# Kernel optimization log

Hardware: AMD Instinct MI355X
Metric: run time of the kernel (lower is better)

The kernel has to match this reference:

```python
import jax, jax.numpy as jnp
import numpy as np

B, S, D, H = 4, 2048, 1024, 16
HD = D // H  # head_dim = 64


def setup_inputs() -> dict:
    key = jax.random.key(0)
    ks = jax.random.split(key, 6)
    sd = 1.0 / np.sqrt(D)
    return {
        "x": jax.random.normal(ks[0], (B, S, D), dtype=jnp.float32),
        "y": jax.random.normal(ks[1], (B, S, D), dtype=jnp.float32),
        "mask": jax.random.normal(ks[2], (1, 1, S, S), dtype=jnp.float32),
        "Wkv": jax.random.normal(ks[3], (D, 2 * D), dtype=jnp.float32) * sd,
        "bkv": jnp.zeros((2 * D,), dtype=jnp.float32),
        "Wq": jax.random.normal(ks[4], (D, D), dtype=jnp.float32) * sd,
        "bq": jnp.zeros((D,), dtype=jnp.float32),
        "Wo": jax.random.normal(ks[5], (D, D), dtype=jnp.float32) * sd,
        "bo": jnp.zeros((D,), dtype=jnp.float32),
    }


def reference(x, y, mask, Wkv, bkv, Wq, bq, Wo, bo):
    b, s, d = x.shape
    kv = x @ Wkv + bkv                      # [B,S,2D]
    q = y @ Wq + bq                         # [B,S,D]
    kv = kv.reshape(b, s, H, 2 * HD).transpose(0, 2, 1, 3)  # [B,H,S,2HD]
    q = q.reshape(b, s, H, HD).transpose(0, 2, 1, 3)        # [B,H,S,HD]
    k, v = kv[..., :HD], kv[..., HD:]
    scaled = jnp.einsum("bhqd,bhkd->bhqk", q, k) / jnp.sqrt(jnp.float32(HD))
    scaled = scaled + mask                  # additive mask, broadcast [1,1,S,S]
    attn = jax.nn.softmax(scaled, axis=-1)
    vals = jnp.einsum("bhqk,bhkd->bhqd", attn, v)  # [B,H,S,HD]
    vals = vals.transpose(0, 2, 1, 3).reshape(b, s, d)
    return vals @ Wo + bo
```

## Files before the change

kernel.cpp:

```cpp
#include <hip/hip_runtime.h>

#define LOG2E 1.44269504088896340736f
#define QSCALE 0.18033688011112042f

typedef __attribute__((ext_vector_type(8))) short bf16x8;
typedef __attribute__((ext_vector_type(4))) float f32x4;

__device__ __forceinline__ unsigned short f2b(float f) {
  union { float f; unsigned int u; } x; x.f = f;
  return (unsigned short)((x.u + 0x8000u) >> 16);
}

__device__ __forceinline__ unsigned int pk_bf16(float a, float b) {
  union { float f; unsigned int u; } xa, xb; xa.f = a; xb.f = b;
  return __builtin_amdgcn_perm(xb.u + 0x8000u, xa.u + 0x8000u, 0x07060302);
}

__device__ __forceinline__ void gld_lds16(const void* g, void* l) {
  __builtin_amdgcn_global_load_lds((const __attribute__((address_space(1))) void*)g,
                                   (__attribute__((address_space(3))) void*)l,
                                   16, 0, 0);
}

__global__ __launch_bounds__(256) void cast_xy(const float* __restrict__ x,
                                               const float* __restrict__ y,
                                               unsigned short* __restrict__ xb,
                                               unsigned short* __restrict__ yb) {
  int i = blockIdx.x * 256 + threadIdx.x;
  const float* in = x; unsigned short* out = xb;
  if (i >= 2097152) { in = y; out = yb; i -= 2097152; }
  float4 v = ((const float4*)in)[i];
  uint2 o;
  o.x = pk_bf16(v.x, v.y);
  o.y = pk_bf16(v.z, v.w);
  ((uint2*)out)[i] = o;
}

__global__ __launch_bounds__(256) void scale_mask(const float* __restrict__ in,
                                                  float* __restrict__ out) {
  int i = blockIdx.x * 256 + threadIdx.x;
  f32x4 v = ((const f32x4*)in)[i];
  ((f32x4*)out)[i] = v * LOG2E;
}

__global__ __launch_bounds__(256) void transpose_cast_all(
    const float* __restrict__ Wkv, const float* __restrict__ Wq,
    const float* __restrict__ Wo, unsigned short* __restrict__ wkvt,
    unsigned short* __restrict__ wqt, unsigned short* __restrict__ wot) {
  __shared__ float t[32][33];
  int tb = blockIdx.x;
  const float* W; unsigned short* Wt; int N;
  if (tb < 2048)      { W = Wkv; Wt = wkvt; N = 2048; }
  else if (tb < 3072) { W = Wq;  Wt = wqt;  N = 1024; tb -= 2048; }
  else                { W = Wo;  Wt = wot;  N = 1024; tb -= 3072; }
  const int K = 1024;
  int tilesN = N >> 5;
  int nb = (tb % tilesN) * 32, kb = (tb / tilesN) * 32;
  int j = threadIdx.x & 31, i0 = threadIdx.x >> 5;
  #pragma unroll
  for (int p = 0; p < 4; ++p) {
    int i = i0 + p * 8;
    t[i][j] = W[(size_t)(kb + i) * N + nb + j];
  }
  __syncthreads();
  #pragma unroll
  for (int p = 0; p < 4; ++p) {
    int i = i0 + p * 8;
    Wt[(size_t)(nb + i) * K + kb + j] = f2b(t[j][i]);
  }
}

template <int MODE>
__global__ __launch_bounds__(256)
void gemm128(const unsigned short* __restrict__ A,
             const unsigned short* __restrict__ Bt,
             const float* __restrict__ bias,
             void* __restrict__ out0, void* __restrict__ out1,
             int M, int N, int K) {
  __shared__ __align__(16) unsigned short As[128 * 64];
  __shared__ __align__(16) unsigned short Bs[128 * 64];
  const int tid = threadIdx.x;
  const int bn = blockIdx.x, bm = blockIdx.y;
  const int wave = tid >> 6, lane = tid & 63;
  const int wm = (wave >> 1) * 64, wn = (wave & 1) * 64;
  const int lrow = lane & 15, quad = lane >> 4;
  const int sw = lrow & 7;

  f32x4 acc[4][4];
  #pragma unroll
  for (int i = 0; i < 4; ++i)
    #pragma unroll
    for (int j = 0; j < 4; ++j)
      #pragma unroll
      for (int r = 0; r < 4; ++r) acc[i][j][r] = 0.f;

  const unsigned short* Ab = A + (size_t)(bm * 128) * K;
  const unsigned short* Bb = Bt + (size_t)(bn * 128) * K;

  for (int k0 = 0; k0 < K; k0 += 64) {
    #pragma unroll
    for (int i = 0; i < 4; ++i) {
      int e = i * 256 + tid;
      int row = e >> 3, gs = (e & 7) ^ (row & 7);
      gld_lds16(Ab + (size_t)row * K + k0 + gs * 8, &As[e * 8]);
    }
    #pragma unroll
    for (int i = 0; i < 4; ++i) {
      int e = i * 256 + tid;
      int row = e >> 3, gs = (e & 7) ^ (row & 7);
      gld_lds16(Bb + (size_t)row * K + k0 + gs * 8, &Bs[e * 8]);
    }
    __builtin_amdgcn_s_waitcnt(0);
    __syncthreads();
    #pragma unroll
    for (int ks = 0; ks < 2; ++ks) {
      bf16x8 af[4], bf[4];
      const int g = ((ks * 4 + quad) ^ sw) * 8;
      #pragma unroll
      for (int i = 0; i < 4; ++i)
        af[i] = *(const bf16x8*)&As[(wm + i * 16 + lrow) * 64 + g];
      #pragma unroll
      for (int j = 0; j < 4; ++j)
        bf[j] = *(const bf16x8*)&Bs[(wn + j * 16 + lrow) * 64 + g];
      #pragma unroll
      for (int i = 0; i < 4; ++i)
        #pragma unroll
        for (int j = 0; j < 4; ++j)
          acc[i][j] = __builtin_amdgcn_mfma_f32_16x16x32_bf16(af[i], bf[j], acc[i][j], 0, 0, 0);
    }
    __syncthreads();
  }

  const int col0 = bn * 128 + wn;
  #pragma unroll
  for (int i = 0; i < 4; ++i) {
    const int row0 = bm * 128 + wm + i * 16 + quad * 4;
    const int b = row0 >> 11, s0 = row0 & 2047;
    #pragma unroll
    for (int j = 0; j < 4; ++j) {
      const int cc = j * 16 + lrow;
      const float bv = bias[col0 + cc];
      float v0 = acc[i][j][0] + bv, v1 = acc[i][j][1] + bv;
      float v2 = acc[i][j][2] + bv, v3 = acc[i][j][3] + bv;
      if (MODE == 0) {
        float* C = (float*)out0;
        size_t off = (size_t)row0 * N + col0 + cc;
        C[off] = v0; C[off + N] = v1; C[off + 2 * N] = v2; C[off + 3 * N] = v3;
      } else if (MODE == 1) {
        const int h = col0 >> 7;
        if ((col0 & 64) == 0) {
          unsigned short* Kb = (unsigned short*)out0;
          size_t base = ((size_t)(b * 16 + h) * 2048 + s0) * 64 + cc;
          Kb[base] = f2b(v0); Kb[base + 64] = f2b(v1);
          Kb[base + 128] = f2b(v2); Kb[base + 192] = f2b(v3);
        } else {
          unsigned short* Vt = (unsigned short*)out1;
          size_t base = ((size_t)(b * 16 + h) * 64 + cc) * 2048 + s0;
          uint2 p; p.x = pk_bf16(v0, v1); p.y = pk_bf16(v2, v3);
          *(uint2*)&Vt[base] = p;
        }
      } else {
        v0 *= QSCALE; v1 *= QSCALE; v2 *= QSCALE; v3 *= QSCALE;
        const int h = col0 >> 6;
        unsigned short* Qb = (unsigned short*)out0;
        size_t base = ((size_t)(b * 16 + h) * 2048 + s0) * 64 + cc;
        Qb[base] = f2b(v0); Qb[base + 64] = f2b(v1);
        Qb[base + 128] = f2b(v2); Qb[base + 192] = f2b(v3);
      }
    }
  }
}

__global__ __launch_bounds__(256)
void attn(const unsigned short* __restrict__ Qbuf,
          const unsigned short* __restrict__ Kbuf,
          const unsigned short* __restrict__ Vtbuf,
          const float* __restrict__ masks,
          unsigned short* __restrict__ vals) {
  const int blk = blockIdx.x;
  const int xcd = blk & 7, slot = blk >> 3;
  const int qt = xcd * 2 + (slot >> 6);
  const int hb = slot & 63;
  const int b = hb >> 4, h = hb & 15;
  const int tid = threadIdx.x, lane = tid & 63, w = tid >> 6;
  const int lrow = lane & 15, quad = lane >> 4;
  const int sw = lrow & 7;

  __shared__ __align__(16) unsigned short Ks[64 * 64];
  __shared__ __align__(16) unsigned short Vs[64 * 64];
  __shared__ __align__(16) unsigned short Ps[128 * 72];

  const unsigned short* qp = Qbuf + ((size_t)(b * 16 + h) * 2048 + qt * 128) * 64;
  const unsigned short* kp = Kbuf + (size_t)(b * 16 + h) * 2048 * 64;
  const unsigned short* vp = Vtbuf + (size_t)(b * 16 + h) * 64 * 2048;
  const float* mp = masks + (size_t)(qt * 128 + w * 32) * 2048;

  #pragma unroll
  for (int i = 0; i < 4; ++i) {
    int e = i * 256 + tid;
    int row = e >> 3, gs = (e & 7) ^ (row & 7);
    gld_lds16(qp + (size_t)row * 64 + gs * 8, &Ps[e * 8]);
  }
  __builtin_amdgcn_s_waitcnt(0);
  __syncthreads();
  bf16x8 qf[2][2];
  #pragma unroll
  for (int iq = 0; iq < 2; ++iq)
    #pragma unroll
    for (int ks = 0; ks < 2; ++ks)
      qf[iq][ks] = *(const bf16x8*)&Ps[(w * 32 + iq * 16 + lrow) * 64 + ((ks * 4 + quad) ^ sw) * 8];
  __syncthreads();

  f32x4 o_acc[4][2];
  #pragma unroll
  for (int id = 0; id < 4; ++id)
    #pragma unroll
    for (int iq = 0; iq < 2; ++iq)
      #pragma unroll
      for (int r = 0; r < 4; ++r) o_acc[id][iq][r] = 0.f;
  float lsum[2] = {0.f, 0.f};

  for (int kt = 0; kt < 32; ++kt) {
    __syncthreads();
    #pragma unroll
    for (int i = 0; i < 2; ++i) {
      int e = i * 256 + tid;
      int row = e >> 3, gs = (e & 7) ^ (row & 7);
      gld_lds16(kp + (size_t)(kt * 64 + row) * 64 + gs * 8, &Ks[e * 8]);
    }
    #pragma unroll
    for (int i = 0; i < 2; ++i) {
      int e = i * 256 + tid;
      int row = e >> 3, gs = (e & 7) ^ (row & 7);
      gld_lds16(vp + (size_t)row * 2048 + kt * 64 + gs * 8, &Vs[e * 8]);
    }
    __builtin_amdgcn_s_waitcnt(0);
    __syncthreads();

    f32x4 z[4][2];
    #pragma unroll
    for (int ik = 0; ik < 4; ++ik)
      #pragma unroll
      for (int iq = 0; iq < 2; ++iq)
        z[ik][iq] = *(const f32x4*)(mp + (size_t)(iq * 16 + lrow) * 2048 + kt * 64 + ik * 16 + quad * 4);

    #pragma unroll
    for (int ks = 0; ks < 2; ++ks) {
      bf16x8 kf[4];
      const int g = ((ks * 4 + quad) ^ sw) * 8;
      #pragma unroll
      for (int ik = 0; ik < 4; ++ik)
        kf[ik] = *(const bf16x8*)&Ks[(ik * 16 + lrow) * 64 + g];
      #pragma unroll
      for (int ik = 0; ik < 4; ++ik)
        #pragma unroll
        for (int iq = 0; iq < 2; ++iq)
          z[ik][iq] = __builtin_amdgcn_mfma_f32_16x16x32_bf16(kf[ik], qf[iq][ks], z[ik][iq], 0, 0, 0);
    }

    #pragma unroll
    for (int ik = 0; ik < 4; ++ik)
      #pragma unroll
      for (int iq = 0; iq < 2; ++iq) {
        float e0 = exp2f(z[ik][iq][0]), e1 = exp2f(z[ik][iq][1]);
        float e2 = exp2f(z[ik][iq][2]), e3 = exp2f(z[ik][iq][3]);
        lsum[iq] += (e0 + e1) + (e2 + e3);
        uint2 p;
        p.x = pk_bf16(e0, e1);
        p.y = pk_bf16(e2, e3);
        *(uint2*)&Ps[(w * 32 + iq * 16 + lrow) * 72 + ik * 16 + quad * 4] = p;
      }
    __builtin_amdgcn_s_waitcnt(0xC07F);

    #pragma unroll
    for (int ks = 0; ks < 2; ++ks) {
      bf16x8 vf[4], pf[2];
      const int g = ((ks * 4 + quad) ^ sw) * 8;
      #pragma unroll
      for (int id = 0; id < 4; ++id)
        vf[id] = *(const bf16x8*)&Vs[(id * 16 + lrow) * 64 + g];
      #pragma unroll
      for (int iq = 0; iq < 2; ++iq)
        pf[iq] = *(const bf16x8*)&Ps[(w * 32 + iq * 16 + lrow) * 72 + ks * 32 + quad * 8];
      #pragma unroll
      for (int id = 0; id < 4; ++id)
        #pragma unroll
        for (int iq = 0; iq < 2; ++iq)
          o_acc[id][iq] = __builtin_amdgcn_mfma_f32_16x16x32_bf16(vf[id], pf[iq], o_acc[id][iq], 0, 0, 0);
    }
  }

  unsigned short* ob = vals + (size_t)(b * 2048 + qt * 128 + w * 32) * 1024 + h * 64;
  #pragma unroll
  for (int iq = 0; iq < 2; ++iq) {
    float s = lsum[iq];
    s += __shfl_xor(s, 16);
    s += __shfl_xor(s, 32);
    float inv = 1.f / s;
    #pragma unroll
    for (int id = 0; id < 4; ++id) {
      uint2 p;
      p.x = pk_bf16(o_acc[id][iq][0] * inv, o_acc[id][iq][1] * inv);
      p.y = pk_bf16(o_acc[id][iq][2] * inv, o_acc[id][iq][3] * inv);
      *(uint2*)&ob[(size_t)(iq * 16 + lrow) * 1024 + id * 16 + quad * 4] = p;
    }
  }
}

extern "C" void kernel_launch(void* const* d_in, const int* in_sizes, int n_in,
                              void* d_out, int out_size, void* d_ws, size_t ws_size,
                              hipStream_t stream) {
  const float* x    = (const float*)d_in[0];
  const float* y    = (const float*)d_in[1];
  const float* mask = (const float*)d_in[2];
  const float* Wkv  = (const float*)d_in[3];
  const float* bkv  = (const float*)d_in[4];
  const float* Wq   = (const float*)d_in[5];
  const float* bq   = (const float*)d_in[6];
  const float* Wo   = (const float*)d_in[7];
  const float* bo   = (const float*)d_in[8];

  char* ws = (char*)d_ws;
  unsigned short* xb    = (unsigned short*)(ws + ((size_t)0 << 20));
  unsigned short* yb    = (unsigned short*)(ws + ((size_t)16 << 20));
  unsigned short* wkvt  = (unsigned short*)(ws + ((size_t)32 << 20));
  unsigned short* wqt   = (unsigned short*)(ws + ((size_t)36 << 20));
  unsigned short* wot   = (unsigned short*)(ws + ((size_t)38 << 20));
  unsigned short* kbuf  = (unsigned short*)(ws + ((size_t)40 << 20));
  unsigned short* vtbuf = (unsigned short*)(ws + ((size_t)56 << 20));
  unsigned short* qbuf  = (unsigned short*)(ws + ((size_t)72 << 20));
  unsigned short* valsb = (unsigned short*)(ws + ((size_t)88 << 20));
  float*          masks = (float*)        (ws + ((size_t)108 << 20));

  cast_xy<<<16384, 256, 0, stream>>>(x, y, xb, yb);
  scale_mask<<<4096, 256, 0, stream>>>(mask, masks);
  transpose_cast_all<<<4096, 256, 0, stream>>>(Wkv, Wq, Wo, wkvt, wqt, wot);

  gemm128<1><<<dim3(16, 64), 256, 0, stream>>>(xb, wkvt, bkv, kbuf, vtbuf, 8192, 2048, 1024);
  gemm128<2><<<dim3(8, 64), 256, 0, stream>>>(yb, wqt, bq, qbuf, nullptr, 8192, 1024, 1024);
  attn<<<1024, 256, 0, stream>>>(qbuf, kbuf, vtbuf, masks, valsb);
  gemm128<0><<<dim3(8, 64), 256, 0, stream>>>(valsb, wot, bo, (float*)d_out, nullptr, 8192, 1024, 1024);
}
```

Measured before the change: 466.2 us.

## Double-buffer K tiles and prefetch next K/V during attention compute

The attention loop now issues the next K tile into a second LDS buffer and the next V tile right after the PV MFMAs, so global-to-LDS loads overlap with compute instead of stalling at the top of each iteration. Full syncthreads and waitcnt(0) are replaced by raw s_barrier plus vmcnt/lgkmcnt waits tuned to the outstanding load count. The P staging buffer drops its padding in favour of an XOR swizzle, and launch bounds request 4 blocks per CU. This risks fragile vmcnt counting (mask loads share the counter) and extra register pressure.

```diff
diff --git a/kernel.cpp b/kernel.cpp
--- a/kernel.cpp
+++ b/kernel.cpp
@@ -21,6 +21,13 @@
                                    (__attribute__((address_space(3))) void*)l,
                                    16, 0, 0);
 }
+
+__device__ __forceinline__ void wgbar() {
+  asm volatile("" ::: "memory");
+  __builtin_amdgcn_s_barrier();
+  asm volatile("" ::: "memory");
+}
+#define SWAIT(s) asm volatile("s_waitcnt " s ::: "memory")
 
 __global__ __launch_bounds__(256) void cast_xy(const float* __restrict__ x,
                                                const float* __restrict__ y,
@@ -171,7 +178,7 @@
   }
 }
 
-__global__ __launch_bounds__(256)
+__global__ __launch_bounds__(256, 4)
 void attn(const unsigned short* __restrict__ Qbuf,
           const unsigned short* __restrict__ Kbuf,
           const unsigned short* __restrict__ Vtbuf,
@@ -186,9 +193,9 @@
   const int lrow = lane & 15, quad = lane >> 4;
   const int sw = lrow & 7;
 
-  __shared__ __align__(16) unsigned short Ks[64 * 64];
+  __shared__ __align__(16) unsigned short Ks[2][64 * 64];
   __shared__ __align__(16) unsigned short Vs[64 * 64];
-  __shared__ __align__(16) unsigned short Ps[128 * 72];
+  __shared__ __align__(16) unsigned short Ps[128 * 64];
 
   const unsigned short* qp = Qbuf + ((size_t)(b * 16 + h) * 2048 + qt * 128) * 64;
   const unsigned short* kp = Kbuf + (size_t)(b * 16 + h) * 2048 * 64;
@@ -201,15 +208,27 @@
     int row = e >> 3, gs = (e & 7) ^ (row & 7);
     gld_lds16(qp + (size_t)row * 64 + gs * 8, &Ps[e * 8]);
   }
-  __builtin_amdgcn_s_waitcnt(0);
-  __syncthreads();
+  #pragma unroll
+  for (int i = 0; i < 2; ++i) {
+    int e = i * 256 + tid;
+    int row = e >> 3, gs = (e & 7) ^ (row & 7);
+    gld_lds16(kp + (size_t)row * 64 + gs * 8, &Ks[0][e * 8]);
+  }
+  #pragma unroll
+  for (int i = 0; i < 2; ++i) {
+    int e = i * 256 + tid;
+    int row = e >> 3, gs = (e & 7) ^ (row & 7);
+    gld_lds16(vp + (size_t)row * 2048 + gs * 8, &Vs[e * 8]);
+  }
+  SWAIT("vmcnt(4)");
+  wgbar();
+
   bf16x8 qf[2][2];
   #pragma unroll
   for (int iq = 0; iq < 2; ++iq)
     #pragma unroll
     for (int ks = 0; ks < 2; ++ks)
       qf[iq][ks] = *(const bf16x8*)&Ps[(w * 32 + iq * 16 + lrow) * 64 + ((ks * 4 + quad) ^ sw) * 8];
-  __syncthreads();
 
   f32x4 o_acc[4][2];
   #pragma unroll
@@ -220,29 +239,27 @@
       for (int r = 0; r < 4; ++r) o_acc[id][iq][r] = 0.f;
   float lsum[2] = {0.f, 0.f};
 
-  for (int kt = 0; kt < 32; ++kt) {
-    __syncthreads();
+  for (int t = 0; t < 32; ++t) {
+    unsigned short* Kc = &Ks[t & 1][0];
+    unsigned short* Kn = &Ks[(t + 1) & 1][0];
+    const int ktn = (t + 1) & 31;
+
+    f32x4 z[4][2];
+    #pragma unroll
+    for (int ik = 0; ik < 4; ++ik)
+      #pragma unroll
+      for (int iq = 0; iq < 2; ++iq)
+        z[ik][iq] = *(const f32x4*)(mp + (size_t)(iq * 16 + lrow) * 2048 + t * 64 + ik * 16 + quad * 4);
+
+    SWAIT("vmcnt(10)");
+    wgbar();
+
     #pragma unroll
     for (int i = 0; i < 2; ++i) {
       int e = i * 256 + tid;
       int row = e >> 3, gs = (e & 7) ^ (row & 7);
-      gld_lds16(kp + (size_t)(kt * 64 + row) * 64 + gs * 8, &Ks[e * 8]);
-    }
-    #pragma unroll
-    for (int i = 0; i < 2; ++i) {
-      int e = i * 256 + tid;
-      int row = e >> 3, gs = (e & 7) ^ (row & 7);
-      gld_lds16(vp + (size_t)row * 2048 + kt * 64 + gs * 8, &Vs[e * 8]);
-    }
-    __builtin_amdgcn_s_waitcnt(0);
-    __syncthreads();
-
-    f32x4 z[4][2];
-    #pragma unroll
-    for (int ik = 0; ik < 4; ++ik)
-      #pragma unroll
-      for (int iq = 0; iq < 2; ++iq)
-        z[ik][iq] = *(const f32x4*)(mp + (size_t)(iq * 16 + lrow) * 2048 + kt * 64 + ik * 16 + quad * 4);
+      gld_lds16(kp + (size_t)(ktn * 64 + row) * 64 + gs * 8, &Kn[e * 8]);
+    }
 
     #pragma unroll
     for (int ks = 0; ks < 2; ++ks) {
@@ -250,7 +267,7 @@
       const int g = ((ks * 4 + quad) ^ sw) * 8;
       #pragma unroll
       for (int ik = 0; ik < 4; ++ik)
-        kf[ik] = *(const bf16x8*)&Ks[(ik * 16 + lrow) * 64 + g];
+        kf[ik] = *(const bf16x8*)&Kc[(ik * 16 + lrow) * 64 + g];
       #pragma unroll
       for (int ik = 0; ik < 4; ++ik)
         #pragma unroll
@@ -268,9 +285,11 @@
         uint2 p;
         p.x = pk_bf16(e0, e1);
         p.y = pk_bf16(e2, e3);
-        *(uint2*)&Ps[(w * 32 + iq * 16 + lrow) * 72 + ik * 16 + quad * 4] = p;
+        *(uint2*)&Ps[(w * 32 + iq * 16 + lrow) * 64 +
+                     ((ik * 2 + (quad >> 1)) ^ sw) * 8 + (quad & 1) * 4] = p;
       }
-    __builtin_amdgcn_s_waitcnt(0xC07F);
+    SWAIT("lgkmcnt(0)");
+    wgbar();
 
     #pragma unroll
     for (int ks = 0; ks < 2; ++ks) {
@@ -281,12 +300,21 @@
         vf[id] = *(const bf16x8*)&Vs[(id * 16 + lrow) * 64 + g];
       #pragma unroll
       for (int iq = 0; iq < 2; ++iq)
-        pf[iq] = *(const bf16x8*)&Ps[(w * 32 + iq * 16 + lrow) * 72 + ks * 32 + quad * 8];
+        pf[iq] = *(const bf16x8*)&Ps[(w * 32 + iq * 16 + lrow) * 64 + g];
       #pragma unroll
       for (int id = 0; id < 4; ++id)
         #pragma unroll
         for (int iq = 0; iq < 2; ++iq)
           o_acc[id][iq] = __builtin_amdgcn_mfma_f32_16x16x32_bf16(vf[id], pf[iq], o_acc[id][iq], 0, 0, 0);
+    }
+
+    wgbar();
+
+    #pragma unroll
+    for (int i = 0; i < 2; ++i) {
+      int e = i * 256 + tid;
+      int row = e >> 3, gs = (e & 7) ^ (row & 7);
+      gld_lds16(vp + (size_t)row * 2048 + ktn * 64 + gs * 8, &Vs[e * 8]);
     }
   }
 
```

After: 440.1 us. -5.6%, faster.

## Double-buffer K/V tiles and prefetch mask into registers in attention loop

Applied to the files above, without the earlier changes.

The attention kernel now double-buffers K and V tiles in LDS and issues global-to-LDS loads for the next tile before computing on the current one. The mask values for the next tile are prefetched into registers with ping-pong sets. It also interleaves the QK MFMAs with the exp/P-store per subtile and swizzles the P buffer instead of padding it. The barrier and wait count are relaxed to one per tile. This is meant to hide global load latency behind MFMA work, at the cost of more LDS, more registers (occupancy hint of 3), and one redundant wrapped prefetch on the last tile.

```diff
diff --git a/kernel.cpp b/kernel.cpp
--- a/kernel.cpp
+++ b/kernel.cpp
@@ -21,6 +21,13 @@
                                    (__attribute__((address_space(3))) void*)l,
                                    16, 0, 0);
 }
+
+__device__ __forceinline__ void wgbar() {
+  asm volatile("" ::: "memory");
+  __builtin_amdgcn_s_barrier();
+  asm volatile("" ::: "memory");
+}
+#define SWAIT(s) asm volatile("s_waitcnt " s ::: "memory")
 
 __global__ __launch_bounds__(256) void cast_xy(const float* __restrict__ x,
                                                const float* __restrict__ y,
@@ -171,7 +178,78 @@
   }
 }
 
-__global__ __launch_bounds__(256)
+
+#define ATTN_TILE(t, ZC, ZN)                                                   \
+  {                                                                            \
+    unsigned short* Kc = &Ks[(t) & 1][0];                                      \
+    unsigned short* Kn = &Ks[((t) + 1) & 1][0];                                \
+    unsigned short* Vc = &Vs[(t) & 1][0];                                      \
+    unsigned short* Vn = &Vs[((t) + 1) & 1][0];                                \
+    const int ktn = ((t) + 1) & 31;        \
+    SWAIT("vmcnt(0)");      \
+    wgbar();                   \
+    _Pragma("unroll")                                                          \
+    for (int i = 0; i < 2; ++i) {                            \
+      int e = i * 256 + tid;                                                   \
+      int row = e >> 3, gs = (e & 7) ^ (row & 7);                              \
+      gld_lds16(kp + (size_t)(ktn * 64 + row) * 64 + gs * 8, &Kn[e * 8]);      \
+    }                                                                          \
+    _Pragma("unroll")                                                          \
+    for (int i = 0; i < 2; ++i) {                            \
+      int e = i * 256 + tid;                                                   \
+      int row = e >> 3, gs = (e & 7) ^ (row & 7);                              \
+      gld_lds16(vp + (size_t)row * 2048 + ktn * 64 + gs * 8, &Vn[e * 8]);      \
+    }                                                                          \
+    _Pragma("unroll")                                                          \
+    for (int iq = 0; iq < 2; ++iq) {                    \
+      const float* mrow =                                                      \
+          mp + (size_t)(iq * 16 + lrow) * 2048 + quad * 4 + ktn * 64;          \
+      ZN[0][iq] = *(const f32x4*)(mrow);                                       \
+      ZN[1][iq] = *(const f32x4*)(mrow + 16);                                  \
+      ZN[2][iq] = *(const f32x4*)(mrow + 32);                                  \
+      ZN[3][iq] = *(const f32x4*)(mrow + 48);                                  \
+    }                                                                          \
+    _Pragma("unroll")                                                          \
+    for (int ik = 0; ik < 4; ++ik) {               \
+      const int krow = (ik * 16 + lrow) * 64;                                  \
+      bf16x8 kf0 = *(const bf16x8*)&Kc[krow + ((quad ^ sw) * 8)];              \
+      bf16x8 kf1 = *(const bf16x8*)&Kc[krow + (((4 + quad) ^ sw) * 8)];        \
+      _Pragma("unroll")                                                        \
+      for (int iq = 0; iq < 2; ++iq) {                                         \
+        f32x4 zz = ZC[ik][iq];                                                 \
+        zz = __builtin_amdgcn_mfma_f32_16x16x32_bf16(kf0, qf[iq][0], zz, 0, 0, 0); \
+        zz = __builtin_amdgcn_mfma_f32_16x16x32_bf16(kf1, qf[iq][1], zz, 0, 0, 0); \
+        float e0 = exp2f(zz[0]), e1 = exp2f(zz[1]);                            \
+        float e2 = exp2f(zz[2]), e3 = exp2f(zz[3]);                            \
+        lsum[iq] += (e0 + e1) + (e2 + e3);                                     \
+        uint2 p;                                                               \
+        p.x = pk_bf16(e0, e1);                                                 \
+        p.y = pk_bf16(e2, e3);                                                 \
+        *(uint2*)&Ps[(w * 32 + iq * 16 + lrow) * 64 +                          \
+                     ((ik * 2 + (quad >> 1)) ^ sw) * 8 + (quad & 1) * 4] = p;  \
+      }                                                                        \
+    }                                                                          \
+    SWAIT("lgkmcnt(0)");          \
+    _Pragma("unroll")                                                          \
+    for (int ks = 0; ks < 2; ++ks) {                       \
+      bf16x8 vf[4], pf[2];                                                     \
+      const int g = ((ks * 4 + quad) ^ sw) * 8;                                \
+      _Pragma("unroll")                                                        \
+      for (int id = 0; id < 4; ++id)                                           \
+        vf[id] = *(const bf16x8*)&Vc[(id * 16 + lrow) * 64 + g];               \
+      _Pragma("unroll")                                                        \
+      for (int iq = 0; iq < 2; ++iq)                                           \
+        pf[iq] = *(const bf16x8*)&Ps[(w * 32 + iq * 16 + lrow) * 64 + g];      \
+      _Pragma("unroll")                                                        \
+      for (int id = 0; id < 4; ++id)                                           \
+        _Pragma("unroll")                                                      \
+        for (int iq = 0; iq < 2; ++iq)                                         \
+          o_acc[id][iq] = __builtin_amdgcn_mfma_f32_16x16x32_bf16(             \
+              vf[id], pf[iq], o_acc[id][iq], 0, 0, 0);                         \
+    }                                                                          \
+  }
+
+__global__ __launch_bounds__(256, 3)
 void attn(const unsigned short* __restrict__ Qbuf,
           const unsigned short* __restrict__ Kbuf,
           const unsigned short* __restrict__ Vtbuf,
@@ -186,9 +264,9 @@
   const int lrow = lane & 15, quad = lane >> 4;
   const int sw = lrow & 7;
 
-  __shared__ __align__(16) unsigned short Ks[64 * 64];
-  __shared__ __align__(16) unsigned short Vs[64 * 64];
-  __shared__ __align__(16) unsigned short Ps[128 * 72];
+  __shared__ __align__(16) unsigned short Ks[2][64 * 64];
+  __shared__ __align__(16) unsigned short Vs[2][64 * 64];
+  __shared__ __align__(16) unsigned short Ps[128 * 64];
 
   const unsigned short* qp = Qbuf + ((size_t)(b * 16 + h) * 2048 + qt * 128) * 64;
   const unsigned short* kp = Kbuf + (size_t)(b * 16 + h) * 2048 * 64;
@@ -201,15 +279,36 @@
     int row = e >> 3, gs = (e & 7) ^ (row & 7);
     gld_lds16(qp + (size_t)row * 64 + gs * 8, &Ps[e * 8]);
   }
-  __builtin_amdgcn_s_waitcnt(0);
-  __syncthreads();
+  #pragma unroll
+  for (int i = 0; i < 2; ++i) {
+    int e = i * 256 + tid;
+    int row = e >> 3, gs = (e & 7) ^ (row & 7);
+    gld_lds16(kp + (size_t)row * 64 + gs * 8, &Ks[0][e * 8]);
+  }
+  #pragma unroll
+  for (int i = 0; i < 2; ++i) {
+    int e = i * 256 + tid;
+    int row = e >> 3, gs = (e & 7) ^ (row & 7);
+    gld_lds16(vp + (size_t)row * 2048 + gs * 8, &Vs[0][e * 8]);
+  }
+  f32x4 zm0[4][2], zm1[4][2];
+  #pragma unroll
+  for (int iq = 0; iq < 2; ++iq) {
+    const float* mrow = mp + (size_t)(iq * 16 + lrow) * 2048 + quad * 4;
+    zm0[0][iq] = *(const f32x4*)(mrow);
+    zm0[1][iq] = *(const f32x4*)(mrow + 16);
+    zm0[2][iq] = *(const f32x4*)(mrow + 32);
+    zm0[3][iq] = *(const f32x4*)(mrow + 48);
+  }
+  SWAIT("vmcnt(0)");
+  wgbar();
+
   bf16x8 qf[2][2];
   #pragma unroll
   for (int iq = 0; iq < 2; ++iq)
     #pragma unroll
     for (int ks = 0; ks < 2; ++ks)
       qf[iq][ks] = *(const bf16x8*)&Ps[(w * 32 + iq * 16 + lrow) * 64 + ((ks * 4 + quad) ^ sw) * 8];
-  __syncthreads();
 
   f32x4 o_acc[4][2];
   #pragma unroll
@@ -220,74 +319,9 @@
       for (int r = 0; r < 4; ++r) o_acc[id][iq][r] = 0.f;
   float lsum[2] = {0.f, 0.f};
 
-  for (int kt = 0; kt < 32; ++kt) {
-    __syncthreads();
-    #pragma unroll
-    for (int i = 0; i < 2; ++i) {
-      int e = i * 256 + tid;
-      int row = e >> 3, gs = (e & 7) ^ (row & 7);
-      gld_lds16(kp + (size_t)(kt * 64 + row) * 64 + gs * 8, &Ks[e * 8]);
-    }
-    #pragma unroll
-    for (int i = 0; i < 2; ++i) {
-      int e = i * 256 + tid;
-      int row = e >> 3, gs = (e & 7) ^ (row & 7);
-      gld_lds16(vp + (size_t)row * 2048 + kt * 64 + gs * 8, &Vs[e * 8]);
-    }
-    __builtin_amdgcn_s_waitcnt(0);
-    __syncthreads();
-
-    f32x4 z[4][2];
-    #pragma unroll
-    for (int ik = 0; ik < 4; ++ik)
-      #pragma unroll
-      for (int iq = 0; iq < 2; ++iq)
-        z[ik][iq] = *(const f32x4*)(mp + (size_t)(iq * 16 + lrow) * 2048 + kt * 64 + ik * 16 + quad * 4);
-
-    #pragma unroll
-    for (int ks = 0; ks < 2; ++ks) {
-      bf16x8 kf[4];
-      const int g = ((ks * 4 + quad) ^ sw) * 8;
-      #pragma unroll
-      for (int ik = 0; ik < 4; ++ik)
-        kf[ik] = *(const bf16x8*)&Ks[(ik * 16 + lrow) * 64 + g];
-      #pragma unroll
-      for (int ik = 0; ik < 4; ++ik)
-        #pragma unroll
-        for (int iq = 0; iq < 2; ++iq)
-          z[ik][iq] = __builtin_amdgcn_mfma_f32_16x16x32_bf16(kf[ik], qf[iq][ks], z[ik][iq], 0, 0, 0);
-    }
-
-    #pragma unroll
-    for (int ik = 0; ik < 4; ++ik)
-      #pragma unroll
-      for (int iq = 0; iq < 2; ++iq) {
-        float e0 = exp2f(z[ik][iq][0]), e1 = exp2f(z[ik][iq][1]);
-        float e2 = exp2f(z[ik][iq][2]), e3 = exp2f(z[ik][iq][3]);
-        lsum[iq] += (e0 + e1) + (e2 + e3);
-        uint2 p;
-        p.x = pk_bf16(e0, e1);
-        p.y = pk_bf16(e2, e3);
-        *(uint2*)&Ps[(w * 32 + iq * 16 + lrow) * 72 + ik * 16 + quad * 4] = p;
-      }
-    __builtin_amdgcn_s_waitcnt(0xC07F);
-
-    #pragma unroll
-    for (int ks = 0; ks < 2; ++ks) {
-      bf16x8 vf[4], pf[2];
-      const int g = ((ks * 4 + quad) ^ sw) * 8;
-      #pragma unroll
-      for (int id = 0; id < 4; ++id)
-        vf[id] = *(const bf16x8*)&Vs[(id * 16 + lrow) * 64 + g];
-      #pragma unroll
-      for (int iq = 0; iq < 2; ++iq)
-        pf[iq] = *(const bf16x8*)&Ps[(w * 32 + iq * 16 + lrow) * 72 + ks * 32 + quad * 8];
-      #pragma unroll
-      for (int id = 0; id < 4; ++id)
-        #pragma unroll
-        for (int iq = 0; iq < 2; ++iq)
-          o_acc[id][iq] = __builtin_amdgcn_mfma_f32_16x16x32_bf16(vf[id], pf[iq], o_acc[id][iq], 0, 0, 0);
-    }
+  for (int t2 = 0; t2 < 16; ++t2) {
+    ATTN_TILE(2 * t2,     zm0, zm1);
+    ATTN_TILE(2 * t2 + 1, zm1, zm0);
   }
 
   unsigned short* ob = vals + (size_t)(b * 2048 + qt * 128 + w * 32) * 1024 + h * 64;
```

After: 456.3 us. 1.02x faster.

## Restructure attention kernel with double-buffered 32-key tiles and 512 threads

Applied to the files above, without the earlier changes.

Rewrites the attention kernel to use 512 threads (8 waves, 16 query rows each) with 32-key tiles double-buffered in LDS. Each thread issues one async global-to-LDS copy per tile, with K loaded by half the waves and V by the other half, overlapping the next tile's load with compute through a single barrier per tile. The separate mask-scaling pass is removed and the LOG2E scale is folded into the attention kernel's mask load. The cost is more barriers (64 tiles instead of 32), smaller MFMA work per barrier, and reliance on hand-placed waitcnt asm for correctness.

```diff
diff --git a/kernel.cpp b/kernel.cpp
--- a/kernel.cpp
+++ b/kernel.cpp
@@ -21,6 +21,14 @@
                                    (__attribute__((address_space(3))) void*)l,
                                    16, 0, 0);
 }
+
+__device__ __forceinline__ void wgbar() {
+  asm volatile("" ::: "memory");
+  __builtin_amdgcn_s_barrier();
+  asm volatile("" ::: "memory");
+}
+#define SWAIT(s) asm volatile("s_waitcnt " s ::: "memory")
+#define FENCE    asm volatile("" ::: "memory")
 
 __global__ __launch_bounds__(256) void cast_xy(const float* __restrict__ x,
                                                const float* __restrict__ y,
@@ -34,13 +42,6 @@
   o.x = pk_bf16(v.x, v.y);
   o.y = pk_bf16(v.z, v.w);
   ((uint2*)out)[i] = o;
-}
-
-__global__ __launch_bounds__(256) void scale_mask(const float* __restrict__ in,
-                                                  float* __restrict__ out) {
-  int i = blockIdx.x * 256 + threadIdx.x;
-  f32x4 v = ((const f32x4*)in)[i];
-  ((f32x4*)out)[i] = v * LOG2E;
 }
 
 __global__ __launch_bounds__(256) void transpose_cast_all(
@@ -171,11 +172,60 @@
   }
 }
 
-__global__ __launch_bounds__(256)
+
+#define ATTN_TILE(T, C)                                                        \
+  {                                                                            \
+    const int ktn = ((T) + 1) & 63;        \
+    const float* mr = mp + (size_t)lrow * 2048 + (T) * 32 + quad * 4;          \
+    f32x4 zl0 = *(const f32x4*)(mr);                                           \
+    f32x4 zl1 = *(const f32x4*)(mr + 16);                                      \
+    SWAIT("vmcnt(2)");            \
+    wgbar();                   \
+    gld_lds16(sptr + (size_t)ktn * sstep, (C) ? sdst0 : sdst1);                \
+    const unsigned short* Kc = &Ks[(C)][0];                                    \
+    const unsigned short* Vc = &Vs[(C)][0];                                    \
+    bf16x8 kf00 = *(const bf16x8*)&Kc[lrow * 64 + ((quad ^ sw7) * 8)];         \
+    bf16x8 kf01 = *(const bf16x8*)&Kc[lrow * 64 + (((4 + quad) ^ sw7) * 8)];   \
+    bf16x8 kf10 = *(const bf16x8*)&Kc[(16 + lrow) * 64 + ((quad ^ sw7) * 8)];  \
+    bf16x8 kf11 = *(const bf16x8*)&Kc[(16 + lrow) * 64 + (((4 + quad) ^ sw7) * 8)]; \
+    f32x4 z0 = zl0 * LOG2E, z1 = zl1 * LOG2E;                                  \
+    z0 = __builtin_amdgcn_mfma_f32_16x16x32_bf16(kf00, qf0, z0, 0, 0, 0);      \
+    z0 = __builtin_amdgcn_mfma_f32_16x16x32_bf16(kf01, qf1, z0, 0, 0, 0);      \
+    z1 = __builtin_amdgcn_mfma_f32_16x16x32_bf16(kf10, qf0, z1, 0, 0, 0);      \
+    z1 = __builtin_amdgcn_mfma_f32_16x16x32_bf16(kf11, qf1, z1, 0, 0, 0);      \
+    {                                                                          \
+      float e0 = exp2f(z0[0]), e1 = exp2f(z0[1]);                              \
+      float e2 = exp2f(z0[2]), e3 = exp2f(z0[3]);                              \
+      lsum += (e0 + e1) + (e2 + e3);                                           \
+      uint2 pp; pp.x = pk_bf16(e0, e1); pp.y = pk_bf16(e2, e3);                \
+      *(uint2*)&Ph[pw + (((quad >> 1) ^ sw3) * 8) + ph4] = pp;                 \
+    }                                                                          \
+    {                                                                          \
+      float e0 = exp2f(z1[0]), e1 = exp2f(z1[1]);                              \
+      float e2 = exp2f(z1[2]), e3 = exp2f(z1[3]);                              \
+      lsum += (e0 + e1) + (e2 + e3);                                           \
+      uint2 pp; pp.x = pk_bf16(e0, e1); pp.y = pk_bf16(e2, e3);                \
+      *(uint2*)&Ph[pw + (((2 + (quad >> 1)) ^ sw3) * 8) + ph4] = pp;           \
+    }                                                                          \
+    SWAIT("lgkmcnt(0)");          \
+    {                                                                          \
+      bf16x8 pf = *(const bf16x8*)&Ph[pw + ((quad ^ sw3) * 8)];                \
+      bf16x8 vf0 = *(const bf16x8*)&Vc[lrow * 32 + ((quad ^ sw3) * 8)];        \
+      bf16x8 vf1 = *(const bf16x8*)&Vc[(16 + lrow) * 32 + ((quad ^ sw3) * 8)]; \
+      bf16x8 vf2 = *(const bf16x8*)&Vc[(32 + lrow) * 32 + ((quad ^ sw3) * 8)]; \
+      bf16x8 vf3 = *(const bf16x8*)&Vc[(48 + lrow) * 32 + ((quad ^ sw3) * 8)]; \
+      o_acc0 = __builtin_amdgcn_mfma_f32_16x16x32_bf16(vf0, pf, o_acc0, 0, 0, 0); \
+      o_acc1 = __builtin_amdgcn_mfma_f32_16x16x32_bf16(vf1, pf, o_acc1, 0, 0, 0); \
+      o_acc2 = __builtin_amdgcn_mfma_f32_16x16x32_bf16(vf2, pf, o_acc2, 0, 0, 0); \
+      o_acc3 = __builtin_amdgcn_mfma_f32_16x16x32_bf16(vf3, pf, o_acc3, 0, 0, 0); \
+    }                                                                          \
+  }
+
+__global__ __launch_bounds__(512, 8)
 void attn(const unsigned short* __restrict__ Qbuf,
           const unsigned short* __restrict__ Kbuf,
           const unsigned short* __restrict__ Vtbuf,
-          const float* __restrict__ masks,
+          const float* __restrict__ mask,
           unsigned short* __restrict__ vals) {
   const int blk = blockIdx.x;
   const int xcd = blk & 7, slot = blk >> 3;
@@ -184,126 +234,68 @@
   const int b = hb >> 4, h = hb & 15;
   const int tid = threadIdx.x, lane = tid & 63, w = tid >> 6;
   const int lrow = lane & 15, quad = lane >> 4;
-  const int sw = lrow & 7;
-
-  __shared__ __align__(16) unsigned short Ks[64 * 64];
-  __shared__ __align__(16) unsigned short Vs[64 * 64];
-  __shared__ __align__(16) unsigned short Ps[128 * 72];
+  const int sw7 = lrow & 7, sw3 = lrow & 3;
+
+  __shared__ __align__(16) unsigned short Ks[2][32 * 64];
+  __shared__ __align__(16) unsigned short Vs[2][64 * 32];
+  __shared__ __align__(16) unsigned short Ph[8 * 512];
 
   const unsigned short* qp = Qbuf + ((size_t)(b * 16 + h) * 2048 + qt * 128) * 64;
   const unsigned short* kp = Kbuf + (size_t)(b * 16 + h) * 2048 * 64;
   const unsigned short* vp = Vtbuf + (size_t)(b * 16 + h) * 64 * 2048;
-  const float* mp = masks + (size_t)(qt * 128 + w * 32) * 2048;
-
-  #pragma unroll
-  for (int i = 0; i < 4; ++i) {
-    int e = i * 256 + tid;
-    int row = e >> 3, gs = (e & 7) ^ (row & 7);
-    gld_lds16(qp + (size_t)row * 64 + gs * 8, &Ps[e * 8]);
-  }
-  __builtin_amdgcn_s_waitcnt(0);
-  __syncthreads();
-  bf16x8 qf[2][2];
-  #pragma unroll
-  for (int iq = 0; iq < 2; ++iq)
-    #pragma unroll
-    for (int ks = 0; ks < 2; ++ks)
-      qf[iq][ks] = *(const bf16x8*)&Ps[(w * 32 + iq * 16 + lrow) * 64 + ((ks * 4 + quad) ^ sw) * 8];
-  __syncthreads();
-
-  f32x4 o_acc[4][2];
-  #pragma unroll
-  for (int id = 0; id < 4; ++id)
-    #pragma unroll
-    for (int iq = 0; iq < 2; ++iq)
-      #pragma unroll
-      for (int r = 0; r < 4; ++r) o_acc[id][iq][r] = 0.f;
-  float lsum[2] = {0.f, 0.f};
-
-  for (int kt = 0; kt < 32; ++kt) {
-    __syncthreads();
-    #pragma unroll
-    for (int i = 0; i < 2; ++i) {
-      int e = i * 256 + tid;
-      int row = e >> 3, gs = (e & 7) ^ (row & 7);
-      gld_lds16(kp + (size_t)(kt * 64 + row) * 64 + gs * 8, &Ks[e * 8]);
-    }
-    #pragma unroll
-    for (int i = 0; i < 2; ++i) {
-      int e = i * 256 + tid;
-      int row = e >> 3, gs = (e & 7) ^ (row & 7);
-      gld_lds16(vp + (size_t)row * 2048 + kt * 64 + gs * 8, &Vs[e * 8]);
-    }
-    __builtin_amdgcn_s_waitcnt(0);
-    __syncthreads();
-
-    f32x4 z[4][2];
-    #pragma unroll
-    for (int ik = 0; ik < 4; ++ik)
-      #pragma unroll
-      for (int iq = 0; iq < 2; ++iq)
-        z[ik][iq] = *(const f32x4*)(mp + (size_t)(iq * 16 + lrow) * 2048 + kt * 64 + ik * 16 + quad * 4);
-
-    #pragma unroll
-    for (int ks = 0; ks < 2; ++ks) {
-      bf16x8 kf[4];
-      const int g = ((ks * 4 + quad) ^ sw) * 8;
-      #pragma unroll
-      for (int ik = 0; ik < 4; ++ik)
-        kf[ik] = *(const bf16x8*)&Ks[(ik * 16 + lrow) * 64 + g];
-      #pragma unroll
-      for (int ik = 0; ik < 4; ++ik)
-        #pragma unroll
-        for (int iq = 0; iq < 2; ++iq)
-          z[ik][iq] = __builtin_amdgcn_mfma_f32_16x16x32_bf16(kf[ik], qf[iq][ks], z[ik][iq], 0, 0, 0);
-    }
-
-    #pragma unroll
-    for (int ik = 0; ik < 4; ++ik)
-      #pragma unroll
-      for (int iq = 0; iq < 2; ++iq) {
-        float e0 = exp2f(z[ik][iq][0]), e1 = exp2f(z[ik][iq][1]);
-        float e2 = exp2f(z[ik][iq][2]), e3 = exp2f(z[ik][iq][3]);
-        lsum[iq] += (e0 + e1) + (e2 + e3);
-        uint2 p;
-        p.x = pk_bf16(e0, e1);
-        p.y = pk_bf16(e2, e3);
-        *(uint2*)&Ps[(w * 32 + iq * 16 + lrow) * 72 + ik * 16 + quad * 4] = p;
-      }
-    __builtin_amdgcn_s_waitcnt(0xC07F);
-
-    #pragma unroll
-    for (int ks = 0; ks < 2; ++ks) {
-      bf16x8 vf[4], pf[2];
-      const int g = ((ks * 4 + quad) ^ sw) * 8;
-      #pragma unroll
-      for (int id = 0; id < 4; ++id)
-        vf[id] = *(const bf16x8*)&Vs[(id * 16 + lrow) * 64 + g];
-      #pragma unroll
-      for (int iq = 0; iq < 2; ++iq)
-        pf[iq] = *(const bf16x8*)&Ps[(w * 32 + iq * 16 + lrow) * 72 + ks * 32 + quad * 8];
-      #pragma unroll
-      for (int id = 0; id < 4; ++id)
-        #pragma unroll
-        for (int iq = 0; iq < 2; ++iq)
-          o_acc[id][iq] = __builtin_amdgcn_mfma_f32_16x16x32_bf16(vf[id], pf[iq], o_acc[id][iq], 0, 0, 0);
-    }
-  }
-
-  unsigned short* ob = vals + (size_t)(b * 2048 + qt * 128 + w * 32) * 1024 + h * 64;
-  #pragma unroll
-  for (int iq = 0; iq < 2; ++iq) {
-    float s = lsum[iq];
-    s += __shfl_xor(s, 16);
-    s += __shfl_xor(s, 32);
-    float inv = 1.f / s;
-    #pragma unroll
-    for (int id = 0; id < 4; ++id) {
-      uint2 p;
-      p.x = pk_bf16(o_acc[id][iq][0] * inv, o_acc[id][iq][1] * inv);
-      p.y = pk_bf16(o_acc[id][iq][2] * inv, o_acc[id][iq][3] * inv);
-      *(uint2*)&ob[(size_t)(iq * 16 + lrow) * 1024 + id * 16 + quad * 4] = p;
-    }
+  const float* mp = mask + (size_t)(qt * 128 + w * 16) * 2048;
+
+  const unsigned short* sptr; int sstep;
+  unsigned short *sdst0, *sdst1;
+  if (w < 4) {
+    int e = tid, row = e >> 3, g = (e & 7) ^ (row & 7);
+    sptr = kp + row * 64 + g * 8;
+    sstep = 2048;
+    sdst0 = &Ks[0][e * 8]; sdst1 = &Ks[1][e * 8];
+  } else {
+    int e = tid - 256, row = e >> 2, g = (e & 3) ^ (row & 3);
+    sptr = vp + (size_t)row * 2048 + g * 8;
+    sstep = 32;
+    sdst0 = &Vs[0][e * 8]; sdst1 = &Vs[1][e * 8];
+  }
+  const int pw = w * 512 + lrow * 32;
+  const int ph4 = (quad & 1) * 4;
+
+  bf16x8 qf0 = *(const bf16x8*)(qp + (size_t)(w * 16 + lrow) * 64 + quad * 8);
+  bf16x8 qf1 = *(const bf16x8*)(qp + (size_t)(w * 16 + lrow) * 64 + 32 + quad * 8);
+  FENCE;
+  gld_lds16(sptr, sdst0);
+  FENCE;
+
+  f32x4 o_acc0, o_acc1, o_acc2, o_acc3;
+  #pragma unroll
+  for (int r = 0; r < 4; ++r) { o_acc0[r] = 0.f; o_acc1[r] = 0.f; o_acc2[r] = 0.f; o_acc3[r] = 0.f; }
+  float lsum = 0.f;
+
+  for (int tt = 0; tt < 64; tt += 2) {
+    ATTN_TILE(tt, 0);
+    ATTN_TILE(tt + 1, 1);
+  }
+
+  float s = lsum;
+  s += __shfl_xor(s, 16);
+  s += __shfl_xor(s, 32);
+  float inv = 1.f / s;
+  unsigned short* ob = vals + (size_t)(b * 2048 + qt * 128 + w * 16 + lrow) * 1024 + h * 64;
+  {
+    uint2 p;
+    p.x = pk_bf16(o_acc0[0] * inv, o_acc0[1] * inv);
+    p.y = pk_bf16(o_acc0[2] * inv, o_acc0[3] * inv);
+    *(uint2*)&ob[quad * 4] = p;
+    p.x = pk_bf16(o_acc1[0] * inv, o_acc1[1] * inv);
+    p.y = pk_bf16(o_acc1[2] * inv, o_acc1[3] * inv);
+    *(uint2*)&ob[16 + quad * 4] = p;
+    p.x = pk_bf16(o_acc2[0] * inv, o_acc2[1] * inv);
+    p.y = pk_bf16(o_acc2[2] * inv, o_acc2[3] * inv);
+    *(uint2*)&ob[32 + quad * 4] = p;
+    p.x = pk_bf16(o_acc3[0] * inv, o_acc3[1] * inv);
+    p.y = pk_bf16(o_acc3[2] * inv, o_acc3[3] * inv);
+    *(uint2*)&ob[48 + quad * 4] = p;
   }
 }
 
@@ -330,14 +322,12 @@
   unsigned short* vtbuf = (unsigned short*)(ws + ((size_t)56 << 20));
   unsigned short* qbuf  = (unsigned short*)(ws + ((size_t)72 << 20));
   unsigned short* valsb = (unsigned short*)(ws + ((size_t)88 << 20));
-  float*          masks = (float*)        (ws + ((size_t)108 << 20));
 
   cast_xy<<<16384, 256, 0, stream>>>(x, y, xb, yb);
-  scale_mask<<<4096, 256, 0, stream>>>(mask, masks);
   transpose_cast_all<<<4096, 256, 0, stream>>>(Wkv, Wq, Wo, wkvt, wqt, wot);
 
   gemm128<1><<<dim3(16, 64), 256, 0, stream>>>(xb, wkvt, bkv, kbuf, vtbuf, 8192, 2048, 1024);
   gemm128<2><<<dim3(8, 64), 256, 0, stream>>>(yb, wqt, bq, qbuf, nullptr, 8192, 1024, 1024);
-  attn<<<1024, 256, 0, stream>>>(qbuf, kbuf, vtbuf, masks, valsb);
+  attn<<<1024, 512, 0, stream>>>(qbuf, kbuf, vtbuf, mask, valsb);
   gemm128<0><<<dim3(8, 64), 256, 0, stream>>>(valsb, wot, bo, (float*)d_out, nullptr, 8192, 1024, 1024);
 }
```

Result: slower. 573.8 us (+23.1%).
